# Kernel optimization log

Hardware: AMD Instinct MI355X
Metric: run time of the kernel (lower is better)

Reference implementation:

```python
import jax, jax.numpy as jnp
import numpy as np

N = 100000       # nodes
DEG = 16         # in-degree per node
E = N * DEG      # edges
IN_DIM = 128
H_DIM = 128
NEG_SLOPE = 0.01  # F.leaky_relu default


def setup_inputs() -> dict:
    key = jax.random.key(0)
    ks = jax.random.split(key, 12)
    sc = 0.05
    attr = jax.random.normal(ks[0], (N, IN_DIM), jnp.float32)
    edge_d = jax.random.uniform(ks[1], (E, 1), dtype=jnp.float32)
    edge_src = jax.random.randint(ks[2], (E,), 0, N, dtype=jnp.int32)
    edge_dst = jnp.repeat(jnp.arange(N, dtype=jnp.int32), DEG)  # every node gets DEG msgs
    return {
        "attr": attr,
        "edge_d": edge_d,
        "W_V1": jax.random.normal(ks[3], (1, 1), jnp.float32) * sc,
        "W_W1": jax.random.normal(ks[4], (H_DIM, IN_DIM), jnp.float32) * sc,
        "W_U1": jax.random.normal(ks[5], (H_DIM, IN_DIM), jnp.float32) * sc,
        "W_a1": jax.random.normal(ks[6], (1, 2 * H_DIM + 1), jnp.float32) * sc,
        "W_V2": jax.random.normal(ks[7], (1, 1), jnp.float32) * sc,
        "W_W2": jax.random.normal(ks[8], (H_DIM, H_DIM), jnp.float32) * sc,
        "W_U2": jax.random.normal(ks[9], (H_DIM, H_DIM), jnp.float32) * sc,
        "W_a2": jax.random.normal(ks[10], (1, 2 * H_DIM + 1), jnp.float32) * sc,
        "edge_src": edge_src,
        "edge_dst": edge_dst,
    }


def gat_layer(h, edge_d, edge_src, edge_dst, W_V, W_W, W_U, W_a):
    n = h.shape[0]
    t = edge_d @ W_V.T                      # [E,1] edge feature transform (fcV)
    z = h @ W_W.T                           # [N,H] (fcW)
    z_i = h @ W_U.T                         # [N,H] (fcU)
    Hd = z.shape[1]
    a = W_a[0]                              # [2H+1]
    a_src, a_dst, a_t = a[:Hd], a[Hd:2 * Hd], a[2 * Hd:]
    # attn_fc(concat(z_src, z_dst, t)) decomposed into per-node scores + edge term
    s_src = z @ a_src                       # [N]
    s_dst = z @ a_dst                       # [N]
    e = s_src[edge_src] + s_dst[edge_dst] + (t @ a_t)  # [E]
    e = jax.nn.leaky_relu(e, NEG_SLOPE)
    # per-destination-node softmax over incoming edges (mailbox softmax)
    m = jax.ops.segment_max(e, edge_dst, num_segments=n)
    ex = jnp.exp(e - m[edge_dst])
    denom = jax.ops.segment_sum(ex, edge_dst, num_segments=n)
    alpha = ex / denom[edge_dst]            # [E]
    # weighted neighbor aggregation
    zn = jax.ops.segment_sum(alpha[:, None] * z[edge_src], edge_dst, num_segments=n)
    return jax.nn.relu(z_i + zn)


def reference(attr, edge_d, W_V1, W_W1, W_U1, W_a1, W_V2, W_W2, W_U2, W_a2,
              edge_src, edge_dst):
    h = gat_layer(attr, edge_d, edge_src, edge_dst, W_V1, W_W1, W_U1, W_a1)
    h = gat_layer(h, edge_d, edge_src, edge_dst, W_V2, W_W2, W_U2, W_a2)
    return h
```

## Files before the change

### kernel.cpp

```cpp
#include <hip/hip_runtime.h>

#define N_NODES 100000
#define DEG 16
#define DIM 128
#define NTILES 1563
#define T8 196
#define DGRID (T8 * 4 * 8)
#define LSTR 136

typedef short bf16x8 __attribute__((ext_vector_type(8)));
typedef float f32x4 __attribute__((ext_vector_type(4)));

__device__ __forceinline__ unsigned short f2bf(float f) {
    unsigned int u = __builtin_bit_cast(unsigned int, f);
    u = (u + 0x7fffu + ((u >> 16) & 1u)) >> 16;
    return (unsigned short)u;
}
__device__ __forceinline__ float bf2f(unsigned short h) {
    unsigned int u = ((unsigned int)h) << 16;
    return __builtin_bit_cast(float, u);
}
__device__ __forceinline__ bf16x8 pack_bf16x8(float4 lo, float4 hi) {
    bf16x8 f;
    f[0] = (short)f2bf(lo.x); f[1] = (short)f2bf(lo.y);
    f[2] = (short)f2bf(lo.z); f[3] = (short)f2bf(lo.w);
    f[4] = (short)f2bf(hi.x); f[5] = (short)f2bf(hi.y);
    f[6] = (short)f2bf(hi.z); f[7] = (short)f2bf(hi.w);
    return f;
}

__global__ __launch_bounds__(256) void prep_w(
    const float* __restrict__ W_W1, const float* __restrict__ W_U1,
    const float* __restrict__ W_W2, const float* __restrict__ W_U2,
    unsigned short* __restrict__ Wc1, unsigned short* __restrict__ Wc2)
{
    int idx = blockIdx.x * 256 + threadIdx.x;
    int half = idx & 32767;
    const float* src = (idx < 32768)
        ? (half < 16384 ? W_W1 + half : W_U1 + half - 16384)
        : (half < 16384 ? W_W2 + half : W_U2 + half - 16384);
    unsigned short* dst = (idx < 32768) ? Wc1 + half : Wc2 + half;
    *dst = f2bf(*src);
}

__global__ __launch_bounds__(256, 4) void dense_tile(
    const float* __restrict__ hsrc,
    const unsigned short* __restrict__ Wc,
    const float* __restrict__ W_a,
    unsigned short* __restrict__ z,
    unsigned short* __restrict__ zi,
    float* __restrict__ s_src0, float* __restrict__ s_src1,
    float* __restrict__ s_dst0, float* __restrict__ s_dst1)
{
    __shared__ unsigned short Wt[64 * LSTR];
    __shared__ unsigned short Ht[64 * LSTR];

    const int bid = blockIdx.x;
    const int xcd = bid & 7;
    const int q = bid >> 3;
    const int cb = q & 3;
    const int tile = (q >> 2) * 8 + xcd;
    if (tile >= NTILES) return;
    const int nodebase = tile * 64;
    const int t = threadIdx.x;

    {
        int r = t >> 2, c0 = (t & 3) * 32;
        const unsigned short* src = Wc + (size_t)(cb * 64 + r) * DIM + c0;
        unsigned short* dst = Wt + r * LSTR + c0;
#pragma unroll
        for (int i = 0; i < 4; i++)
            *(uint4*)(dst + i * 8) = *(const uint4*)(src + i * 8);
    }
    {
        int r = t >> 2, c0 = (t & 3) * 32;
        int node = nodebase + r;
        unsigned short* dst = Ht + r * LSTR + c0;
        float4 v[8];
#pragma unroll
        for (int i = 0; i < 8; i++) v[i] = make_float4(0.f, 0.f, 0.f, 0.f);
        if (node < N_NODES) {
            const float* src = hsrc + (size_t)node * DIM + c0;
#pragma unroll
            for (int i = 0; i < 8; i++) v[i] = *(const float4*)(src + i * 4);
        }
#pragma unroll
        for (int i = 0; i < 4; i++)
            *(bf16x8*)(dst + i * 8) = pack_bf16x8(v[2 * i], v[2 * i + 1]);
    }
    __syncthreads();

    const int wave = t >> 6;
    const int lane = t & 63;
    const int n16 = lane & 15;
    const int quad = lane >> 4;
    const int node = nodebase + wave * 16 + n16;

    bf16x8 hfrag[4];
    const unsigned short* hrow = Ht + (wave * 16 + n16) * LSTR + quad * 8;
#pragma unroll
    for (int ks = 0; ks < 4; ks++)
        hfrag[ks] = *(const bf16x8*)(hrow + ks * 32);

    f32x4 acc[4];
#pragma unroll
    for (int ct = 0; ct < 4; ct++) {
        const unsigned short* wrow = Wt + (ct * 16 + n16) * LSTR + quad * 8;
        f32x4 a = {0.f, 0.f, 0.f, 0.f};
#pragma unroll
        for (int ks = 0; ks < 4; ks++)
            a = __builtin_amdgcn_mfma_f32_16x16x32_bf16(
                    *(const bf16x8*)(wrow + ks * 32), hfrag[ks], a, 0, 0, 0);
        acc[ct] = a;
    }

    if (node < N_NODES) {
        unsigned short* zout = (cb < 2 ? z : zi);
        unsigned short* orow = zout + (size_t)node * DIM + (cb & 1) * 64 + quad * 4;
#pragma unroll
        for (int ct = 0; ct < 4; ct++) {
            uint2 pk;
            pk.x = (unsigned int)f2bf(acc[ct][0]) | ((unsigned int)f2bf(acc[ct][1]) << 16);
            pk.y = (unsigned int)f2bf(acc[ct][2]) | ((unsigned int)f2bf(acc[ct][3]) << 16);
            *(uint2*)(orow + ct * 16) = pk;
        }
    }

    if (cb < 2) {
        float ps = 0.f, pd = 0.f;
#pragma unroll
        for (int ct = 0; ct < 4; ct++) {
            float4 as = *(const float4*)(W_a + cb * 64 + ct * 16 + quad * 4);
            float4 ad = *(const float4*)(W_a + DIM + cb * 64 + ct * 16 + quad * 4);
            ps += acc[ct][0] * as.x + acc[ct][1] * as.y
                + acc[ct][2] * as.z + acc[ct][3] * as.w;
            pd += acc[ct][0] * ad.x + acc[ct][1] * ad.y
                + acc[ct][2] * ad.z + acc[ct][3] * ad.w;
        }
        ps += __shfl_xor(ps, 16); ps += __shfl_xor(ps, 32);
        pd += __shfl_xor(pd, 16); pd += __shfl_xor(pd, 32);
        if (lane < 16 && node < N_NODES) {
            (cb == 0 ? s_src0 : s_src1)[node] = ps;
            (cb == 0 ? s_dst0 : s_dst1)[node] = pd;
        }
    }
}

__global__ __launch_bounds__(256, 3) void aggr_dense(
    const unsigned short* __restrict__ z,
    const unsigned short* __restrict__ zi,
    const float* __restrict__ s_src0, const float* __restrict__ s_src1,
    const float* __restrict__ s_dst0, const float* __restrict__ s_dst1,
    const float* __restrict__ edge_d,
    const int* __restrict__ edge_src,
    const float* __restrict__ W_V,
    const float* __restrict__ W_a,
    const unsigned short* __restrict__ Wc2,
    const float* __restrict__ W_a2,
    unsigned short* __restrict__ z2,
    unsigned short* __restrict__ zi2,
    float* __restrict__ t_src0, float* __restrict__ t_src1,
    float* __restrict__ t_dst0, float* __restrict__ t_dst1)
{
    __shared__ float alpha_s[16][DEG];
    __shared__ int   src_s[16][DEG];
    __shared__ unsigned short Hl[16 * LSTR];

    const int t = threadIdx.x;
    const int base = blockIdx.x * 16;

    {
        int nl = t >> 4, j = t & 15;
        int node = base + nl;
        int e = node * DEG + j;
        int s = edge_src[e];
        float coef = W_V[0] * W_a[2 * DIM];
        float x = (s_src0[s] + s_src1[s]) + (s_dst0[node] + s_dst1[node])
                + edge_d[e] * coef;
        x = x > 0.f ? x : 0.01f * x;
        float m = x;
        m = fmaxf(m, __shfl_xor(m, 1));
        m = fmaxf(m, __shfl_xor(m, 2));
        m = fmaxf(m, __shfl_xor(m, 4));
        m = fmaxf(m, __shfl_xor(m, 8));
        float ex = __expf(x - m);
        float d = ex;
        d += __shfl_xor(d, 1); d += __shfl_xor(d, 2);
        d += __shfl_xor(d, 4); d += __shfl_xor(d, 8);
        alpha_s[nl][j] = ex / d;
        src_s[nl][j] = s;
    }
    __syncthreads();

    {
        const int nl = t >> 4;
        const int node = base + nl;
        const int c8 = (t & 15) * 8;

        uint4 raw[DEG];
#pragma unroll
        for (int j = 0; j < DEG; j++)
            raw[j] = *(const uint4*)(z + (size_t)src_s[nl][j] * DIM + c8);
        uint4 zr = *(const uint4*)(zi + (size_t)node * DIM + c8);

        float acc[8] = {};
#pragma unroll
        for (int j = 0; j < DEG; j++) {
            float a = alpha_s[nl][j];
            acc[0] += a * bf2f((unsigned short)raw[j].x);
            acc[1] += a * bf2f((unsigned short)(raw[j].x >> 16));
            acc[2] += a * bf2f((unsigned short)raw[j].y);
            acc[3] += a * bf2f((unsigned short)(raw[j].y >> 16));
            acc[4] += a * bf2f((unsigned short)raw[j].z);
            acc[5] += a * bf2f((unsigned short)(raw[j].z >> 16));
            acc[6] += a * bf2f((unsigned short)raw[j].w);
            acc[7] += a * bf2f((unsigned short)(raw[j].w >> 16));
        }

        float v[8];
        v[0] = fmaxf(bf2f((unsigned short)zr.x) + acc[0], 0.f);
        v[1] = fmaxf(bf2f((unsigned short)(zr.x >> 16)) + acc[1], 0.f);
        v[2] = fmaxf(bf2f((unsigned short)zr.y) + acc[2], 0.f);
        v[3] = fmaxf(bf2f((unsigned short)(zr.y >> 16)) + acc[3], 0.f);
        v[4] = fmaxf(bf2f((unsigned short)zr.z) + acc[4], 0.f);
        v[5] = fmaxf(bf2f((unsigned short)(zr.z >> 16)) + acc[5], 0.f);
        v[6] = fmaxf(bf2f((unsigned short)zr.w) + acc[6], 0.f);
        v[7] = fmaxf(bf2f((unsigned short)(zr.w >> 16)) + acc[7], 0.f);

        uint4 pk;
        pk.x = (unsigned int)f2bf(v[0]) | ((unsigned int)f2bf(v[1]) << 16);
        pk.y = (unsigned int)f2bf(v[2]) | ((unsigned int)f2bf(v[3]) << 16);
        pk.z = (unsigned int)f2bf(v[4]) | ((unsigned int)f2bf(v[5]) << 16);
        pk.w = (unsigned int)f2bf(v[6]) | ((unsigned int)f2bf(v[7]) << 16);
        *(uint4*)(Hl + nl * LSTR + c8) = pk;
    }
    __syncthreads();

    const int wave = t >> 6;
    const int lane = t & 63;
    const int n16 = lane & 15;
    const int quad = lane >> 4;
    const int node = base + n16;

    bf16x8 hfrag[4];
    const unsigned short* hrow = Hl + n16 * LSTR + quad * 8;
#pragma unroll
    for (int ks = 0; ks < 4; ks++)
        hfrag[ks] = *(const bf16x8*)(hrow + ks * 32);

    f32x4 acc[4];
#pragma unroll
    for (int ct = 0; ct < 4; ct++) {
        const unsigned short* wrow = Wc2 + (size_t)(wave * 64 + ct * 16 + n16) * DIM + quad * 8;
        f32x4 a = {0.f, 0.f, 0.f, 0.f};
#pragma unroll
        for (int ks = 0; ks < 4; ks++)
            a = __builtin_amdgcn_mfma_f32_16x16x32_bf16(
                    *(const bf16x8*)(wrow + ks * 32), hfrag[ks], a, 0, 0, 0);
        acc[ct] = a;
    }

    {
        unsigned short* zout = (wave < 2 ? z2 : zi2);
        unsigned short* orow = zout + (size_t)node * DIM + (wave & 1) * 64 + quad * 4;
#pragma unroll
        for (int ct = 0; ct < 4; ct++) {
            uint2 pk;
            pk.x = (unsigned int)f2bf(acc[ct][0]) | ((unsigned int)f2bf(acc[ct][1]) << 16);
            pk.y = (unsigned int)f2bf(acc[ct][2]) | ((unsigned int)f2bf(acc[ct][3]) << 16);
            *(uint2*)(orow + ct * 16) = pk;
        }
    }

    if (wave < 2) {
        float ps = 0.f, pd = 0.f;
#pragma unroll
        for (int ct = 0; ct < 4; ct++) {
            float4 as = *(const float4*)(W_a2 + wave * 64 + ct * 16 + quad * 4);
            float4 ad = *(const float4*)(W_a2 + DIM + wave * 64 + ct * 16 + quad * 4);
            ps += acc[ct][0] * as.x + acc[ct][1] * as.y
                + acc[ct][2] * as.z + acc[ct][3] * as.w;
            pd += acc[ct][0] * ad.x + acc[ct][1] * ad.y
                + acc[ct][2] * ad.z + acc[ct][3] * ad.w;
        }
        ps += __shfl_xor(ps, 16); ps += __shfl_xor(ps, 32);
        pd += __shfl_xor(pd, 16); pd += __shfl_xor(pd, 32);
        if (lane < 16) {
            (wave == 0 ? t_src0 : t_src1)[node] = ps;
            (wave == 0 ? t_dst0 : t_dst1)[node] = pd;
        }
    }
}

__global__ __launch_bounds__(256, 3) void aggr_final(
    const unsigned short* __restrict__ z,
    const unsigned short* __restrict__ zi,
    const float* __restrict__ s_src0, const float* __restrict__ s_src1,
    const float* __restrict__ s_dst0, const float* __restrict__ s_dst1,
    const float* __restrict__ edge_d,
    const int* __restrict__ edge_src,
    const float* __restrict__ W_V,
    const float* __restrict__ W_a,
    float* __restrict__ out_f32)
{
    __shared__ float alpha_s[16][DEG];
    __shared__ int   src_s[16][DEG];

    const int t = threadIdx.x;
    const int base = blockIdx.x * 16;

    {
        int nl = t >> 4, j = t & 15;
        int node = base + nl;
        int e = node * DEG + j;
        int s = edge_src[e];
        float coef = W_V[0] * W_a[2 * DIM];
        float x = (s_src0[s] + s_src1[s]) + (s_dst0[node] + s_dst1[node])
                + edge_d[e] * coef;
        x = x > 0.f ? x : 0.01f * x;
        float m = x;
        m = fmaxf(m, __shfl_xor(m, 1));
        m = fmaxf(m, __shfl_xor(m, 2));
        m = fmaxf(m, __shfl_xor(m, 4));
        m = fmaxf(m, __shfl_xor(m, 8));
        float ex = __expf(x - m);
        float d = ex;
        d += __shfl_xor(d, 1); d += __shfl_xor(d, 2);
        d += __shfl_xor(d, 4); d += __shfl_xor(d, 8);
        alpha_s[nl][j] = ex / d;
        src_s[nl][j] = s;
    }
    __syncthreads();

    const int nl = t >> 4;
    const int node = base + nl;
    const int c8 = (t & 15) * 8;

    uint4 raw[DEG];
#pragma unroll
    for (int j = 0; j < DEG; j++)
        raw[j] = *(const uint4*)(z + (size_t)src_s[nl][j] * DIM + c8);
    uint4 zr = *(const uint4*)(zi + (size_t)node * DIM + c8);

    float acc[8] = {};
#pragma unroll
    for (int j = 0; j < DEG; j++) {
        float a = alpha_s[nl][j];
        acc[0] += a * bf2f((unsigned short)raw[j].x);
        acc[1] += a * bf2f((unsigned short)(raw[j].x >> 16));
        acc[2] += a * bf2f((unsigned short)raw[j].y);
        acc[3] += a * bf2f((unsigned short)(raw[j].y >> 16));
        acc[4] += a * bf2f((unsigned short)raw[j].z);
        acc[5] += a * bf2f((unsigned short)(raw[j].z >> 16));
        acc[6] += a * bf2f((unsigned short)raw[j].w);
        acc[7] += a * bf2f((unsigned short)(raw[j].w >> 16));
    }

    float* op = out_f32 + (size_t)node * DIM + c8;
    *(float4*)op = make_float4(
        fmaxf(bf2f((unsigned short)zr.x) + acc[0], 0.f),
        fmaxf(bf2f((unsigned short)(zr.x >> 16)) + acc[1], 0.f),
        fmaxf(bf2f((unsigned short)zr.y) + acc[2], 0.f),
        fmaxf(bf2f((unsigned short)(zr.y >> 16)) + acc[3], 0.f));
    *(float4*)(op + 4) = make_float4(
        fmaxf(bf2f((unsigned short)zr.z) + acc[4], 0.f),
        fmaxf(bf2f((unsigned short)(zr.z >> 16)) + acc[5], 0.f),
        fmaxf(bf2f((unsigned short)zr.w) + acc[6], 0.f),
        fmaxf(bf2f((unsigned short)(zr.w >> 16)) + acc[7], 0.f));
}

extern "C" void kernel_launch(void* const* d_in, const int* in_sizes, int n_in,
                              void* d_out, int out_size, void* d_ws, size_t ws_size,
                              hipStream_t stream) {
    const float* attr     = (const float*)d_in[0];
    const float* edge_d   = (const float*)d_in[1];
    const float* W_V1     = (const float*)d_in[2];
    const float* W_W1     = (const float*)d_in[3];
    const float* W_U1     = (const float*)d_in[4];
    const float* W_a1     = (const float*)d_in[5];
    const float* W_V2     = (const float*)d_in[6];
    const float* W_W2     = (const float*)d_in[7];
    const float* W_U2     = (const float*)d_in[8];
    const float* W_a2     = (const float*)d_in[9];
    const int*   edge_src = (const int*)d_in[10];

    float* out = (float*)d_out;

    char* ws = (char*)d_ws;
    unsigned short* z1  = (unsigned short*)ws;
    unsigned short* zi1 = (unsigned short*)(ws + 26u * 1024 * 1024);
    unsigned short* z2  = (unsigned short*)(ws + 52u * 1024 * 1024);
    unsigned short* zi2 = (unsigned short*)(ws + 78u * 1024 * 1024);
    unsigned short* Wc1 = (unsigned short*)(ws + 104u * 1024 * 1024);
    unsigned short* Wc2 = (unsigned short*)(ws + 105u * 1024 * 1024);
    float* s_src0       = (float*)(ws + 106u * 1024 * 1024);
    float* s_src1       = (float*)(ws + 107u * 1024 * 1024);
    float* s_dst0       = (float*)(ws + 108u * 1024 * 1024);
    float* s_dst1       = (float*)(ws + 109u * 1024 * 1024);
    float* t_src0       = (float*)(ws + 110u * 1024 * 1024);
    float* t_src1       = (float*)(ws + 111u * 1024 * 1024);
    float* t_dst0       = (float*)(ws + 112u * 1024 * 1024);
    float* t_dst1       = (float*)(ws + 113u * 1024 * 1024);

    prep_w<<<256, 256, 0, stream>>>(W_W1, W_U1, W_W2, W_U2, Wc1, Wc2);

    dense_tile<<<DGRID, 256, 0, stream>>>(attr, Wc1, W_a1, z1, zi1,
                                          s_src0, s_src1, s_dst0, s_dst1);

    aggr_dense<<<6250, 256, 0, stream>>>(z1, zi1, s_src0, s_src1, s_dst0, s_dst1,
                                         edge_d, edge_src, W_V1, W_a1,
                                         Wc2, W_a2, z2, zi2,
                                         t_src0, t_src1, t_dst0, t_dst1);

    aggr_final<<<6250, 256, 0, stream>>>(z2, zi2, t_src0, t_src1, t_dst0, t_dst1,
                                         edge_d, edge_src, W_V2, W_a2, out);
}
```

Measured before the change: 326.0 us.

## Issue neighbor gathers before softmax using wave shuffles instead of LDS staging

In both aggregation kernels, the per-edge source indices and softmax weights are now passed between lanes with wave shuffles rather than written to shared memory behind a block barrier. The 16 neighbor-row gathers and the self-row load are issued right after the edge indices are read, and a scheduling barrier keeps them ahead of the attention-score and softmax arithmetic so that arithmetic runs while the loads are in flight. This removes the shared-memory round trip and one __syncthreads per block. In exchange, each thread keeps more registers live across the softmax, which could lower occupancy.

```diff
diff --git a/kernel.cpp b/kernel.cpp
--- a/kernel.cpp
+++ b/kernel.cpp
@@ -162,71 +162,75 @@
     float* __restrict__ t_src0, float* __restrict__ t_src1,
     float* __restrict__ t_dst0, float* __restrict__ t_dst1)
 {
-    __shared__ float alpha_s[16][DEG];
-    __shared__ int   src_s[16][DEG];
     __shared__ unsigned short Hl[16 * LSTR];
 
     const int t = threadIdx.x;
     const int base = blockIdx.x * 16;
+    const int nl = t >> 4;
+    const int j  = t & 15;
+    const int nodej = base + nl;
+    const int lane = t & 63;
+    const int gb = lane & 48;
+
+    const int e = nodej * DEG + j;
+
+    int   s  = edge_src[e];
+    float ed = edge_d[e];
+
+    float v_ss0 = s_src0[s];
+    float v_ss1 = s_src1[s];
+    float v_sd0 = s_dst0[nodej];
+    float v_sd1 = s_dst1[nodej];
+
+    const int c8 = j * 8;
+    uint4 raw[DEG];
+#pragma unroll
+    for (int jj = 0; jj < DEG; jj++) {
+        int sj = __shfl(s, gb | jj);
+        raw[jj] = *(const uint4*)(z + (size_t)sj * DIM + c8);
+    }
+    uint4 zr = *(const uint4*)(zi + (size_t)nodej * DIM + c8);
+    __builtin_amdgcn_sched_barrier(0);
+
+    float coef = W_V[0] * W_a[2 * DIM];
+    float x = (v_ss0 + v_ss1) + (v_sd0 + v_sd1) + ed * coef;
+    x = x > 0.f ? x : 0.01f * x;
+    float m = x;
+    m = fmaxf(m, __shfl_xor(m, 1));
+    m = fmaxf(m, __shfl_xor(m, 2));
+    m = fmaxf(m, __shfl_xor(m, 4));
+    m = fmaxf(m, __shfl_xor(m, 8));
+    float ex = __expf(x - m);
+    float d = ex;
+    d += __shfl_xor(d, 1); d += __shfl_xor(d, 2);
+    d += __shfl_xor(d, 4); d += __shfl_xor(d, 8);
+    float aj = ex / d;
+
+    float acc8[8] = {};
+#pragma unroll
+    for (int jj = 0; jj < DEG; jj++) {
+        float a = __shfl(aj, gb | jj);
+        acc8[0] += a * bf2f((unsigned short)raw[jj].x);
+        acc8[1] += a * bf2f((unsigned short)(raw[jj].x >> 16));
+        acc8[2] += a * bf2f((unsigned short)raw[jj].y);
+        acc8[3] += a * bf2f((unsigned short)(raw[jj].y >> 16));
+        acc8[4] += a * bf2f((unsigned short)raw[jj].z);
+        acc8[5] += a * bf2f((unsigned short)(raw[jj].z >> 16));
+        acc8[6] += a * bf2f((unsigned short)raw[jj].w);
+        acc8[7] += a * bf2f((unsigned short)(raw[jj].w >> 16));
+    }
+
+    float v[8];
+    v[0] = fmaxf(bf2f((unsigned short)zr.x) + acc8[0], 0.f);
+    v[1] = fmaxf(bf2f((unsigned short)(zr.x >> 16)) + acc8[1], 0.f);
+    v[2] = fmaxf(bf2f((unsigned short)zr.y) + acc8[2], 0.f);
+    v[3] = fmaxf(bf2f((unsigned short)(zr.y >> 16)) + acc8[3], 0.f);
+    v[4] = fmaxf(bf2f((unsigned short)zr.z) + acc8[4], 0.f);
+    v[5] = fmaxf(bf2f((unsigned short)(zr.z >> 16)) + acc8[5], 0.f);
+    v[6] = fmaxf(bf2f((unsigned short)zr.w) + acc8[6], 0.f);
+    v[7] = fmaxf(bf2f((unsigned short)(zr.w >> 16)) + acc8[7], 0.f);
 
     {
-        int nl = t >> 4, j = t & 15;
-        int node = base + nl;
-        int e = node * DEG + j;
-        int s = edge_src[e];
-        float coef = W_V[0] * W_a[2 * DIM];
-        float x = (s_src0[s] + s_src1[s]) + (s_dst0[node] + s_dst1[node])
-                + edge_d[e] * coef;
-        x = x > 0.f ? x : 0.01f * x;
-        float m = x;
-        m = fmaxf(m, __shfl_xor(m, 1));
-        m = fmaxf(m, __shfl_xor(m, 2));
-        m = fmaxf(m, __shfl_xor(m, 4));
-        m = fmaxf(m, __shfl_xor(m, 8));
-        float ex = __expf(x - m);
-        float d = ex;
-        d += __shfl_xor(d, 1); d += __shfl_xor(d, 2);
-        d += __shfl_xor(d, 4); d += __shfl_xor(d, 8);
-        alpha_s[nl][j] = ex / d;
-        src_s[nl][j] = s;
-    }
-    __syncthreads();
-
-    {
-        const int nl = t >> 4;
-        const int node = base + nl;
-        const int c8 = (t & 15) * 8;
-
-        uint4 raw[DEG];
-#pragma unroll
-        for (int j = 0; j < DEG; j++)
-            raw[j] = *(const uint4*)(z + (size_t)src_s[nl][j] * DIM + c8);
-        uint4 zr = *(const uint4*)(zi + (size_t)node * DIM + c8);
-
-        float acc[8] = {};
-#pragma unroll
-        for (int j = 0; j < DEG; j++) {
-            float a = alpha_s[nl][j];
-            acc[0] += a * bf2f((unsigned short)raw[j].x);
-            acc[1] += a * bf2f((unsigned short)(raw[j].x >> 16));
-            acc[2] += a * bf2f((unsigned short)raw[j].y);
-            acc[3] += a * bf2f((unsigned short)(raw[j].y >> 16));
-            acc[4] += a * bf2f((unsigned short)raw[j].z);
-            acc[5] += a * bf2f((unsigned short)(raw[j].z >> 16));
-            acc[6] += a * bf2f((unsigned short)raw[j].w);
-            acc[7] += a * bf2f((unsigned short)(raw[j].w >> 16));
-        }
-
-        float v[8];
-        v[0] = fmaxf(bf2f((unsigned short)zr.x) + acc[0], 0.f);
-        v[1] = fmaxf(bf2f((unsigned short)(zr.x >> 16)) + acc[1], 0.f);
-        v[2] = fmaxf(bf2f((unsigned short)zr.y) + acc[2], 0.f);
-        v[3] = fmaxf(bf2f((unsigned short)(zr.y >> 16)) + acc[3], 0.f);
-        v[4] = fmaxf(bf2f((unsigned short)zr.z) + acc[4], 0.f);
-        v[5] = fmaxf(bf2f((unsigned short)(zr.z >> 16)) + acc[5], 0.f);
-        v[6] = fmaxf(bf2f((unsigned short)zr.w) + acc[6], 0.f);
-        v[7] = fmaxf(bf2f((unsigned short)(zr.w >> 16)) + acc[7], 0.f);
-
         uint4 pk;
         pk.x = (unsigned int)f2bf(v[0]) | ((unsigned int)f2bf(v[1]) << 16);
         pk.y = (unsigned int)f2bf(v[2]) | ((unsigned int)f2bf(v[3]) << 16);
@@ -237,7 +241,6 @@
     __syncthreads();
 
     const int wave = t >> 6;
-    const int lane = t & 63;
     const int n16 = lane & 15;
     const int quad = lane >> 4;
     const int node = base + n16;
@@ -303,57 +306,60 @@
     const float* __restrict__ W_a,
     float* __restrict__ out_f32)
 {
-    __shared__ float alpha_s[16][DEG];
-    __shared__ int   src_s[16][DEG];
-
     const int t = threadIdx.x;
     const int base = blockIdx.x * 16;
-
-    {
-        int nl = t >> 4, j = t & 15;
-        int node = base + nl;
-        int e = node * DEG + j;
-        int s = edge_src[e];
-        float coef = W_V[0] * W_a[2 * DIM];
-        float x = (s_src0[s] + s_src1[s]) + (s_dst0[node] + s_dst1[node])
-                + edge_d[e] * coef;
-        x = x > 0.f ? x : 0.01f * x;
-        float m = x;
-        m = fmaxf(m, __shfl_xor(m, 1));
-        m = fmaxf(m, __shfl_xor(m, 2));
-        m = fmaxf(m, __shfl_xor(m, 4));
-        m = fmaxf(m, __shfl_xor(m, 8));
-        float ex = __expf(x - m);
-        float d = ex;
-        d += __shfl_xor(d, 1); d += __shfl_xor(d, 2);
-        d += __shfl_xor(d, 4); d += __shfl_xor(d, 8);
-        alpha_s[nl][j] = ex / d;
-        src_s[nl][j] = s;
-    }
-    __syncthreads();
-
     const int nl = t >> 4;
+    const int j  = t & 15;
     const int node = base + nl;
-    const int c8 = (t & 15) * 8;
-
+    const int lane = t & 63;
+    const int gb = lane & 48;
+
+    const int e = node * DEG + j;
+
+    int   s  = edge_src[e];
+    float ed = edge_d[e];
+
+    float v_ss0 = s_src0[s];
+    float v_ss1 = s_src1[s];
+    float v_sd0 = s_dst0[node];
+    float v_sd1 = s_dst1[node];
+
+    const int c8 = j * 8;
     uint4 raw[DEG];
 #pragma unroll
-    for (int j = 0; j < DEG; j++)
-        raw[j] = *(const uint4*)(z + (size_t)src_s[nl][j] * DIM + c8);
+    for (int jj = 0; jj < DEG; jj++) {
+        int sj = __shfl(s, gb | jj);
+        raw[jj] = *(const uint4*)(z + (size_t)sj * DIM + c8);
+    }
     uint4 zr = *(const uint4*)(zi + (size_t)node * DIM + c8);
+    __builtin_amdgcn_sched_barrier(0);
+
+    float coef = W_V[0] * W_a[2 * DIM];
+    float x = (v_ss0 + v_ss1) + (v_sd0 + v_sd1) + ed * coef;
+    x = x > 0.f ? x : 0.01f * x;
+    float m = x;
+    m = fmaxf(m, __shfl_xor(m, 1));
+    m = fmaxf(m, __shfl_xor(m, 2));
+    m = fmaxf(m, __shfl_xor(m, 4));
+    m = fmaxf(m, __shfl_xor(m, 8));
+    float ex = __expf(x - m);
+    float d = ex;
+    d += __shfl_xor(d, 1); d += __shfl_xor(d, 2);
+    d += __shfl_xor(d, 4); d += __shfl_xor(d, 8);
+    float aj = ex / d;
 
     float acc[8] = {};
 #pragma unroll
-    for (int j = 0; j < DEG; j++) {
-        float a = alpha_s[nl][j];
-        acc[0] += a * bf2f((unsigned short)raw[j].x);
-        acc[1] += a * bf2f((unsigned short)(raw[j].x >> 16));
-        acc[2] += a * bf2f((unsigned short)raw[j].y);
-        acc[3] += a * bf2f((unsigned short)(raw[j].y >> 16));
-        acc[4] += a * bf2f((unsigned short)raw[j].z);
-        acc[5] += a * bf2f((unsigned short)(raw[j].z >> 16));
-        acc[6] += a * bf2f((unsigned short)raw[j].w);
-        acc[7] += a * bf2f((unsigned short)(raw[j].w >> 16));
+    for (int jj = 0; jj < DEG; jj++) {
+        float a = __shfl(aj, gb | jj);
+        acc[0] += a * bf2f((unsigned short)raw[jj].x);
+        acc[1] += a * bf2f((unsigned short)(raw[jj].x >> 16));
+        acc[2] += a * bf2f((unsigned short)raw[jj].y);
+        acc[3] += a * bf2f((unsigned short)(raw[jj].y >> 16));
+        acc[4] += a * bf2f((unsigned short)raw[jj].z);
+        acc[5] += a * bf2f((unsigned short)(raw[jj].z >> 16));
+        acc[6] += a * bf2f((unsigned short)raw[jj].w);
+        acc[7] += a * bf2f((unsigned short)(raw[jj].w >> 16));
     }
 
     float* op = out_f32 + (size_t)node * DIM + c8;
```

Result: no change. 320.0 us (-1.8%).

## Split aggregation into alpha kernel and column-sliced gather, unfuse layer-2 GEMM

Applied to the files above, without the earlier changes.

Replaces the fused aggregate+GEMM kernels with a separate per-edge softmax kernel that writes alpha to memory, a gather kernel where each block handles one 16-column slice of 64 nodes, and a standalone bf16 MFMA GEMM for layer 2. The column slicing, with slice taken from the low bits of blockIdx, is meant to keep each slice of z resident in a smaller cache footprint and raise parallelism for the random gathers. The cost is more launches and extra round-trips to memory for alpha and h1. Launch-bounds occupancy hints are also dropped.

```diff
diff --git a/kernel.cpp b/kernel.cpp
--- a/kernel.cpp
+++ b/kernel.cpp
@@ -3,9 +3,11 @@
 #define N_NODES 100000
 #define DEG 16
 #define DIM 128
+#define E_EDGES 1600000
 #define NTILES 1563
 #define T8 196
 #define DGRID (T8 * 4 * 8)
+#define CHUNKS 1563
 #define LSTR 136
 
 typedef short bf16x8 __attribute__((ext_vector_type(8)));
@@ -43,7 +45,7 @@
     *dst = f2bf(*src);
 }
 
-__global__ __launch_bounds__(256, 4) void dense_tile(
+__global__ __launch_bounds__(256) void dense_tile(
     const float* __restrict__ hsrc,
     const unsigned short* __restrict__ Wc,
     const float* __restrict__ W_a,
@@ -146,227 +148,258 @@
     }
 }
 
-__global__ __launch_bounds__(256, 3) void aggr_dense(
-    const unsigned short* __restrict__ z,
-    const unsigned short* __restrict__ zi,
+__global__ __launch_bounds__(256) void dense_tile_b(
+    const unsigned short* __restrict__ hsrc,
+    const unsigned short* __restrict__ Wc,
+    const float* __restrict__ W_a,
+    unsigned short* __restrict__ z,
+    unsigned short* __restrict__ zi,
+    float* __restrict__ s_src0, float* __restrict__ s_src1,
+    float* __restrict__ s_dst0, float* __restrict__ s_dst1)
+{
+    __shared__ unsigned short Wt[64 * LSTR];
+    __shared__ unsigned short Ht[64 * LSTR];
+
+    const int bid = blockIdx.x;
+    const int xcd = bid & 7;
+    const int q = bid >> 3;
+    const int cb = q & 3;
+    const int tile = (q >> 2) * 8 + xcd;
+    if (tile >= NTILES) return;
+    const int nodebase = tile * 64;
+    const int t = threadIdx.x;
+
+    {
+        int r = t >> 2, c0 = (t & 3) * 32;
+        const unsigned short* src = Wc + (size_t)(cb * 64 + r) * DIM + c0;
+        unsigned short* dst = Wt + r * LSTR + c0;
+#pragma unroll
+        for (int i = 0; i < 4; i++)
+            *(uint4*)(dst + i * 8) = *(const uint4*)(src + i * 8);
+    }
+    {
+        int r = t >> 2, c0 = (t & 3) * 32;
+        int node = nodebase + r;
+        unsigned short* dst = Ht + r * LSTR + c0;
+        if (node < N_NODES) {
+            const unsigned short* src = hsrc + (size_t)node * DIM + c0;
+#pragma unroll
+            for (int i = 0; i < 4; i++)
+                *(uint4*)(dst + i * 8) = *(const uint4*)(src + i * 8);
+        } else {
+            uint4 zr4 = make_uint4(0, 0, 0, 0);
+#pragma unroll
+            for (int i = 0; i < 4; i++) *(uint4*)(dst + i * 8) = zr4;
+        }
+    }
+    __syncthreads();
+
+    const int wave = t >> 6;
+    const int lane = t & 63;
+    const int n16 = lane & 15;
+    const int quad = lane >> 4;
+    const int node = nodebase + wave * 16 + n16;
+
+    bf16x8 hfrag[4];
+    const unsigned short* hrow = Ht + (wave * 16 + n16) * LSTR + quad * 8;
+#pragma unroll
+    for (int ks = 0; ks < 4; ks++)
+        hfrag[ks] = *(const bf16x8*)(hrow + ks * 32);
+
+    f32x4 acc[4];
+#pragma unroll
+    for (int ct = 0; ct < 4; ct++) {
+        const unsigned short* wrow = Wt + (ct * 16 + n16) * LSTR + quad * 8;
+        f32x4 a = {0.f, 0.f, 0.f, 0.f};
+#pragma unroll
+        for (int ks = 0; ks < 4; ks++)
+            a = __builtin_amdgcn_mfma_f32_16x16x32_bf16(
+                    *(const bf16x8*)(wrow + ks * 32), hfrag[ks], a, 0, 0, 0);
+        acc[ct] = a;
+    }
+
+    if (node < N_NODES) {
+        unsigned short* zout = (cb < 2 ? z : zi);
+        unsigned short* orow = zout + (size_t)node * DIM + (cb & 1) * 64 + quad * 4;
+#pragma unroll
+        for (int ct = 0; ct < 4; ct++) {
+            uint2 pk;
+            pk.x = (unsigned int)f2bf(acc[ct][0]) | ((unsigned int)f2bf(acc[ct][1]) << 16);
+            pk.y = (unsigned int)f2bf(acc[ct][2]) | ((unsigned int)f2bf(acc[ct][3]) << 16);
+            *(uint2*)(orow + ct * 16) = pk;
+        }
+    }
+
+    if (cb < 2) {
+        float ps = 0.f, pd = 0.f;
+#pragma unroll
+        for (int ct = 0; ct < 4; ct++) {
+            float4 as = *(const float4*)(W_a + cb * 64 + ct * 16 + quad * 4);
+            float4 ad = *(const float4*)(W_a + DIM + cb * 64 + ct * 16 + quad * 4);
+            ps += acc[ct][0] * as.x + acc[ct][1] * as.y
+                + acc[ct][2] * as.z + acc[ct][3] * as.w;
+            pd += acc[ct][0] * ad.x + acc[ct][1] * ad.y
+                + acc[ct][2] * ad.z + acc[ct][3] * ad.w;
+        }
+        ps += __shfl_xor(ps, 16); ps += __shfl_xor(ps, 32);
+        pd += __shfl_xor(pd, 16); pd += __shfl_xor(pd, 32);
+        if (lane < 16 && node < N_NODES) {
+            (cb == 0 ? s_src0 : s_src1)[node] = ps;
+            (cb == 0 ? s_dst0 : s_dst1)[node] = pd;
+        }
+    }
+}
+
+__global__ __launch_bounds__(256) void alpha_k(
     const float* __restrict__ s_src0, const float* __restrict__ s_src1,
     const float* __restrict__ s_dst0, const float* __restrict__ s_dst1,
     const float* __restrict__ edge_d,
     const int* __restrict__ edge_src,
     const float* __restrict__ W_V,
     const float* __restrict__ W_a,
-    const unsigned short* __restrict__ Wc2,
-    const float* __restrict__ W_a2,
-    unsigned short* __restrict__ z2,
-    unsigned short* __restrict__ zi2,
-    float* __restrict__ t_src0, float* __restrict__ t_src1,
-    float* __restrict__ t_dst0, float* __restrict__ t_dst1)
-{
-    __shared__ float alpha_s[16][DEG];
-    __shared__ int   src_s[16][DEG];
-    __shared__ unsigned short Hl[16 * LSTR];
-
-    const int t = threadIdx.x;
-    const int base = blockIdx.x * 16;
-
-    {
-        int nl = t >> 4, j = t & 15;
-        int node = base + nl;
-        int e = node * DEG + j;
-        int s = edge_src[e];
-        float coef = W_V[0] * W_a[2 * DIM];
-        float x = (s_src0[s] + s_src1[s]) + (s_dst0[node] + s_dst1[node])
-                + edge_d[e] * coef;
-        x = x > 0.f ? x : 0.01f * x;
-        float m = x;
-        m = fmaxf(m, __shfl_xor(m, 1));
-        m = fmaxf(m, __shfl_xor(m, 2));
-        m = fmaxf(m, __shfl_xor(m, 4));
-        m = fmaxf(m, __shfl_xor(m, 8));
-        float ex = __expf(x - m);
-        float d = ex;
-        d += __shfl_xor(d, 1); d += __shfl_xor(d, 2);
-        d += __shfl_xor(d, 4); d += __shfl_xor(d, 8);
-        alpha_s[nl][j] = ex / d;
-        src_s[nl][j] = s;
-    }
-    __syncthreads();
-
-    {
-        const int nl = t >> 4;
-        const int node = base + nl;
-        const int c8 = (t & 15) * 8;
-
-        uint4 raw[DEG];
-#pragma unroll
-        for (int j = 0; j < DEG; j++)
-            raw[j] = *(const uint4*)(z + (size_t)src_s[nl][j] * DIM + c8);
-        uint4 zr = *(const uint4*)(zi + (size_t)node * DIM + c8);
-
-        float acc[8] = {};
-#pragma unroll
-        for (int j = 0; j < DEG; j++) {
-            float a = alpha_s[nl][j];
-            acc[0] += a * bf2f((unsigned short)raw[j].x);
-            acc[1] += a * bf2f((unsigned short)(raw[j].x >> 16));
-            acc[2] += a * bf2f((unsigned short)raw[j].y);
-            acc[3] += a * bf2f((unsigned short)(raw[j].y >> 16));
-            acc[4] += a * bf2f((unsigned short)raw[j].z);
-            acc[5] += a * bf2f((unsigned short)(raw[j].z >> 16));
-            acc[6] += a * bf2f((unsigned short)raw[j].w);
-            acc[7] += a * bf2f((unsigned short)(raw[j].w >> 16));
-        }
-
-        float v[8];
-        v[0] = fmaxf(bf2f((unsigned short)zr.x) + acc[0], 0.f);
-        v[1] = fmaxf(bf2f((unsigned short)(zr.x >> 16)) + acc[1], 0.f);
-        v[2] = fmaxf(bf2f((unsigned short)zr.y) + acc[2], 0.f);
-        v[3] = fmaxf(bf2f((unsigned short)(zr.y >> 16)) + acc[3], 0.f);
-        v[4] = fmaxf(bf2f((unsigned short)zr.z) + acc[4], 0.f);
-        v[5] = fmaxf(bf2f((unsigned short)(zr.z >> 16)) + acc[5], 0.f);
-        v[6] = fmaxf(bf2f((unsigned short)zr.w) + acc[6], 0.f);
-        v[7] = fmaxf(bf2f((unsigned short)(zr.w >> 16)) + acc[7], 0.f);
-
-        uint4 pk;
-        pk.x = (unsigned int)f2bf(v[0]) | ((unsigned int)f2bf(v[1]) << 16);
-        pk.y = (unsigned int)f2bf(v[2]) | ((unsigned int)f2bf(v[3]) << 16);
-        pk.z = (unsigned int)f2bf(v[4]) | ((unsigned int)f2bf(v[5]) << 16);
-        pk.w = (unsigned int)f2bf(v[6]) | ((unsigned int)f2bf(v[7]) << 16);
-        *(uint4*)(Hl + nl * LSTR + c8) = pk;
-    }
-    __syncthreads();
-
-    const int wave = t >> 6;
-    const int lane = t & 63;
-    const int n16 = lane & 15;
-    const int quad = lane >> 4;
-    const int node = base + n16;
-
-    bf16x8 hfrag[4];
-    const unsigned short* hrow = Hl + n16 * LSTR + quad * 8;
-#pragma unroll
-    for (int ks = 0; ks < 4; ks++)
-        hfrag[ks] = *(const bf16x8*)(hrow + ks * 32);
-
-    f32x4 acc[4];
-#pragma unroll
-    for (int ct = 0; ct < 4; ct++) {
-        const unsigned short* wrow = Wc2 + (size_t)(wave * 64 + ct * 16 + n16) * DIM + quad * 8;
-        f32x4 a = {0.f, 0.f, 0.f, 0.f};
-#pragma unroll
-        for (int ks = 0; ks < 4; ks++)
-            a = __builtin_amdgcn_mfma_f32_16x16x32_bf16(
-                    *(const bf16x8*)(wrow + ks * 32), hfrag[ks], a, 0, 0, 0);
-        acc[ct] = a;
-    }
-
-    {
-        unsigned short* zout = (wave < 2 ? z2 : zi2);
-        unsigned short* orow = zout + (size_t)node * DIM + (wave & 1) * 64 + quad * 4;
-#pragma unroll
-        for (int ct = 0; ct < 4; ct++) {
-            uint2 pk;
-            pk.x = (unsigned int)f2bf(acc[ct][0]) | ((unsigned int)f2bf(acc[ct][1]) << 16);
-            pk.y = (unsigned int)f2bf(acc[ct][2]) | ((unsigned int)f2bf(acc[ct][3]) << 16);
-            *(uint2*)(orow + ct * 16) = pk;
-        }
-    }
-
-    if (wave < 2) {
-        float ps = 0.f, pd = 0.f;
-#pragma unroll
-        for (int ct = 0; ct < 4; ct++) {
-            float4 as = *(const float4*)(W_a2 + wave * 64 + ct * 16 + quad * 4);
-            float4 ad = *(const float4*)(W_a2 + DIM + wave * 64 + ct * 16 + quad * 4);
-            ps += acc[ct][0] * as.x + acc[ct][1] * as.y
-                + acc[ct][2] * as.z + acc[ct][3] * as.w;
-            pd += acc[ct][0] * ad.x + acc[ct][1] * ad.y
-                + acc[ct][2] * ad.z + acc[ct][3] * ad.w;
-        }
-        ps += __shfl_xor(ps, 16); ps += __shfl_xor(ps, 32);
-        pd += __shfl_xor(pd, 16); pd += __shfl_xor(pd, 32);
-        if (lane < 16) {
-            (wave == 0 ? t_src0 : t_src1)[node] = ps;
-            (wave == 0 ? t_dst0 : t_dst1)[node] = pd;
-        }
-    }
-}
-
-__global__ __launch_bounds__(256, 3) void aggr_final(
+    float* __restrict__ alpha)
+{
+    const int e = blockIdx.x * 256 + threadIdx.x;
+    const int node = e >> 4;
+    int   s  = edge_src[e];
+    float ed = edge_d[e];
+    float coef = W_V[0] * W_a[2 * DIM];
+    float x = (s_src0[s] + s_src1[s]) + (s_dst0[node] + s_dst1[node]) + ed * coef;
+    x = x > 0.f ? x : 0.01f * x;
+    float m = x;
+    m = fmaxf(m, __shfl_xor(m, 1));
+    m = fmaxf(m, __shfl_xor(m, 2));
+    m = fmaxf(m, __shfl_xor(m, 4));
+    m = fmaxf(m, __shfl_xor(m, 8));
+    float ex = __expf(x - m);
+    float d = ex;
+    d += __shfl_xor(d, 1); d += __shfl_xor(d, 2);
+    d += __shfl_xor(d, 4); d += __shfl_xor(d, 8);
+    alpha[e] = ex / d;
+}
+
+__global__ __launch_bounds__(256) void aggr_slice(
     const unsigned short* __restrict__ z,
     const unsigned short* __restrict__ zi,
-    const float* __restrict__ s_src0, const float* __restrict__ s_src1,
-    const float* __restrict__ s_dst0, const float* __restrict__ s_dst1,
-    const float* __restrict__ edge_d,
+    const float* __restrict__ alpha,
     const int* __restrict__ edge_src,
-    const float* __restrict__ W_V,
-    const float* __restrict__ W_a,
+    unsigned short* __restrict__ hout)
+{
+    __shared__ float alpha_s[64][17];
+    __shared__ int   src_s[64][17];
+
+    const int bid = blockIdx.x;
+    const int slice = bid & 7;
+    const int chunk = bid >> 3;
+    const int t = threadIdx.x;
+    const int nodebase = chunk * 64;
+
+    {
+        int idx = t * 4;
+        int e0 = nodebase * DEG + idx;
+        int nl = idx >> 4, j0 = idx & 15;
+        float4 a4 = make_float4(0.f, 0.f, 0.f, 0.f);
+        int4   s4 = make_int4(0, 0, 0, 0);
+        if (e0 < E_EDGES) {
+            a4 = *(const float4*)(alpha + e0);
+            s4 = *(const int4*)(edge_src + e0);
+        }
+        alpha_s[nl][j0 + 0] = a4.x; alpha_s[nl][j0 + 1] = a4.y;
+        alpha_s[nl][j0 + 2] = a4.z; alpha_s[nl][j0 + 3] = a4.w;
+        src_s[nl][j0 + 0] = s4.x; src_s[nl][j0 + 1] = s4.y;
+        src_s[nl][j0 + 2] = s4.z; src_s[nl][j0 + 3] = s4.w;
+    }
+    __syncthreads();
+
+    const int nl  = t >> 2;
+    const int col = slice * 16 + (t & 3) * 4;
+    const int node = nodebase + nl;
+    const unsigned short* zcol = z + col;
+
+    float a0 = 0.f, a1 = 0.f, a2 = 0.f, a3 = 0.f;
+#pragma unroll
+    for (int e = 0; e < DEG; e++) {
+        int   sj = src_s[nl][e];
+        float a  = alpha_s[nl][e];
+        uint2 r = *(const uint2*)(zcol + (size_t)sj * DIM);
+        a0 += a * bf2f((unsigned short)(r.x & 0xffff));
+        a1 += a * bf2f((unsigned short)(r.x >> 16));
+        a2 += a * bf2f((unsigned short)(r.y & 0xffff));
+        a3 += a * bf2f((unsigned short)(r.y >> 16));
+    }
+
+    if (node < N_NODES) {
+        uint2 zr = *(const uint2*)(zi + (size_t)node * DIM + col);
+        float v0 = fmaxf(bf2f((unsigned short)(zr.x & 0xffff)) + a0, 0.f);
+        float v1 = fmaxf(bf2f((unsigned short)(zr.x >> 16)) + a1, 0.f);
+        float v2 = fmaxf(bf2f((unsigned short)(zr.y & 0xffff)) + a2, 0.f);
+        float v3 = fmaxf(bf2f((unsigned short)(zr.y >> 16)) + a3, 0.f);
+        uint2 pk;
+        pk.x = (unsigned int)f2bf(v0) | ((unsigned int)f2bf(v1) << 16);
+        pk.y = (unsigned int)f2bf(v2) | ((unsigned int)f2bf(v3) << 16);
+        *(uint2*)(hout + (size_t)node * DIM + col) = pk;
+    }
+}
+
+__global__ __launch_bounds__(256) void aggr_slice_final(
+    const unsigned short* __restrict__ z,
+    const unsigned short* __restrict__ zi,
+    const float* __restrict__ alpha,
+    const int* __restrict__ edge_src,
     float* __restrict__ out_f32)
 {
-    __shared__ float alpha_s[16][DEG];
-    __shared__ int   src_s[16][DEG];
-
+    __shared__ float alpha_s[64][17];
+    __shared__ int   src_s[64][17];
+
+    const int bid = blockIdx.x;
+    const int slice = bid & 7;
+    const int chunk = bid >> 3;
     const int t = threadIdx.x;
-    const int base = blockIdx.x * 16;
-
-    {
-        int nl = t >> 4, j = t & 15;
-        int node = base + nl;
-        int e = node * DEG + j;
-        int s = edge_src[e];
-        float coef = W_V[0] * W_a[2 * DIM];
-        float x = (s_src0[s] + s_src1[s]) + (s_dst0[node] + s_dst1[node])
-                + edge_d[e] * coef;
-        x = x > 0.f ? x : 0.01f * x;
-        float m = x;
-        m = fmaxf(m, __shfl_xor(m, 1));
-        m = fmaxf(m, __shfl_xor(m, 2));
-        m = fmaxf(m, __shfl_xor(m, 4));
-        m = fmaxf(m, __shfl_xor(m, 8));
-        float ex = __expf(x - m);
-        float d = ex;
-        d += __shfl_xor(d, 1); d += __shfl_xor(d, 2);
-        d += __shfl_xor(d, 4); d += __shfl_xor(d, 8);
-        alpha_s[nl][j] = ex / d;
-        src_s[nl][j] = s;
+    const int nodebase = chunk * 64;
+
+    {
+        int idx = t * 4;
+        int e0 = nodebase * DEG + idx;
+        int nl = idx >> 4, j0 = idx & 15;
+        float4 a4 = make_float4(0.f, 0.f, 0.f, 0.f);
+        int4   s4 = make_int4(0, 0, 0, 0);
+        if (e0 < E_EDGES) {
+            a4 = *(const float4*)(alpha + e0);
+            s4 = *(const int4*)(edge_src + e0);
+        }
+        alpha_s[nl][j0 + 0] = a4.x; alpha_s[nl][j0 + 1] = a4.y;
+        alpha_s[nl][j0 + 2] = a4.z; alpha_s[nl][j0 + 3] = a4.w;
+        src_s[nl][j0 + 0] = s4.x; src_s[nl][j0 + 1] = s4.y;
+        src_s[nl][j0 + 2] = s4.z; src_s[nl][j0 + 3] = s4.w;
     }
     __syncthreads();
 
-    const int nl = t >> 4;
-    const int node = base + nl;
-    const int c8 = (t & 15) * 8;
-
-    uint4 raw[DEG];
-#pragma unroll
-    for (int j = 0; j < DEG; j++)
-        raw[j] = *(const uint4*)(z + (size_t)src_s[nl][j] * DIM + c8);
-    uint4 zr = *(const uint4*)(zi + (size_t)node * DIM + c8);
-
-    float acc[8] = {};
-#pragma unroll
-    for (int j = 0; j < DEG; j++) {
-        float a = alpha_s[nl][j];
-        acc[0] += a * bf2f((unsigned short)raw[j].x);
-        acc[1] += a * bf2f((unsigned short)(raw[j].x >> 16));
-        acc[2] += a * bf2f((unsigned short)raw[j].y);
-        acc[3] += a * bf2f((unsigned short)(raw[j].y >> 16));
-        acc[4] += a * bf2f((unsigned short)raw[j].z);
-        acc[5] += a * bf2f((unsigned short)(raw[j].z >> 16));
-        acc[6] += a * bf2f((unsigned short)raw[j].w);
-        acc[7] += a * bf2f((unsigned short)(raw[j].w >> 16));
-    }
-
-    float* op = out_f32 + (size_t)node * DIM + c8;
-    *(float4*)op = make_float4(
-        fmaxf(bf2f((unsigned short)zr.x) + acc[0], 0.f),
-        fmaxf(bf2f((unsigned short)(zr.x >> 16)) + acc[1], 0.f),
-        fmaxf(bf2f((unsigned short)zr.y) + acc[2], 0.f),
-        fmaxf(bf2f((unsigned short)(zr.y >> 16)) + acc[3], 0.f));
-    *(float4*)(op + 4) = make_float4(
-        fmaxf(bf2f((unsigned short)zr.z) + acc[4], 0.f),
-        fmaxf(bf2f((unsigned short)(zr.z >> 16)) + acc[5], 0.f),
-        fmaxf(bf2f((unsigned short)zr.w) + acc[6], 0.f),
-        fmaxf(bf2f((unsigned short)(zr.w >> 16)) + acc[7], 0.f));
+    const int nl  = t >> 2;
+    const int col = slice * 16 + (t & 3) * 4;
+    const int node = nodebase + nl;
+    const unsigned short* zcol = z + col;
+
+    float a0 = 0.f, a1 = 0.f, a2 = 0.f, a3 = 0.f;
+#pragma unroll
+    for (int e = 0; e < DEG; e++) {
+        int   sj = src_s[nl][e];
+        float a  = alpha_s[nl][e];
+        uint2 r = *(const uint2*)(zcol + (size_t)sj * DIM);
+        a0 += a * bf2f((unsigned short)(r.x & 0xffff));
+        a1 += a * bf2f((unsigned short)(r.x >> 16));
+        a2 += a * bf2f((unsigned short)(r.y & 0xffff));
+        a3 += a * bf2f((unsigned short)(r.y >> 16));
+    }
+
+    if (node < N_NODES) {
+        uint2 zr = *(const uint2*)(zi + (size_t)node * DIM + col);
+        f32x4 o;
+        o[0] = fmaxf(bf2f((unsigned short)(zr.x & 0xffff)) + a0, 0.f);
+        o[1] = fmaxf(bf2f((unsigned short)(zr.x >> 16)) + a1, 0.f);
+        o[2] = fmaxf(bf2f((unsigned short)(zr.y & 0xffff)) + a2, 0.f);
+        o[3] = fmaxf(bf2f((unsigned short)(zr.y >> 16)) + a3, 0.f);
+        *(f32x4*)(out_f32 + (size_t)node * DIM + col) = o;
+    }
 }
 
 extern "C" void kernel_launch(void* const* d_in, const int* in_sizes, int n_in,
@@ -387,31 +420,34 @@
     float* out = (float*)d_out;
 
     char* ws = (char*)d_ws;
-    unsigned short* z1  = (unsigned short*)ws;
-    unsigned short* zi1 = (unsigned short*)(ws + 26u * 1024 * 1024);
-    unsigned short* z2  = (unsigned short*)(ws + 52u * 1024 * 1024);
-    unsigned short* zi2 = (unsigned short*)(ws + 78u * 1024 * 1024);
-    unsigned short* Wc1 = (unsigned short*)(ws + 104u * 1024 * 1024);
-    unsigned short* Wc2 = (unsigned short*)(ws + 105u * 1024 * 1024);
-    float* s_src0       = (float*)(ws + 106u * 1024 * 1024);
-    float* s_src1       = (float*)(ws + 107u * 1024 * 1024);
-    float* s_dst0       = (float*)(ws + 108u * 1024 * 1024);
-    float* s_dst1       = (float*)(ws + 109u * 1024 * 1024);
-    float* t_src0       = (float*)(ws + 110u * 1024 * 1024);
-    float* t_src1       = (float*)(ws + 111u * 1024 * 1024);
-    float* t_dst0       = (float*)(ws + 112u * 1024 * 1024);
-    float* t_dst1       = (float*)(ws + 113u * 1024 * 1024);
+    unsigned short* z1    = (unsigned short*)ws;
+    unsigned short* zi1   = (unsigned short*)(ws + 26u * 1024 * 1024);
+    unsigned short* h1    = (unsigned short*)(ws + 52u * 1024 * 1024);
+    unsigned short* Wc1   = (unsigned short*)(ws + 78u * 1024 * 1024);
+    unsigned short* Wc2   = (unsigned short*)(ws + 79u * 1024 * 1024);
+    float* s_src0         = (float*)(ws + 80u * 1024 * 1024);
+    float* s_src1         = (float*)(ws + 81u * 1024 * 1024);
+    float* s_dst0         = (float*)(ws + 82u * 1024 * 1024);
+    float* s_dst1         = (float*)(ws + 83u * 1024 * 1024);
+    float* alphaA         = (float*)(ws + 84u * 1024 * 1024);
+    unsigned short* z2  = z1;
+    unsigned short* zi2 = zi1;
 
     prep_w<<<256, 256, 0, stream>>>(W_W1, W_U1, W_W2, W_U2, Wc1, Wc2);
 
     dense_tile<<<DGRID, 256, 0, stream>>>(attr, Wc1, W_a1, z1, zi1,
                                           s_src0, s_src1, s_dst0, s_dst1);
 
-    aggr_dense<<<6250, 256, 0, stream>>>(z1, zi1, s_src0, s_src1, s_dst0, s_dst1,
-                                         edge_d, edge_src, W_V1, W_a1,
-                                         Wc2, W_a2, z2, zi2,
-                                         t_src0, t_src1, t_dst0, t_dst1);
-
-    aggr_final<<<6250, 256, 0, stream>>>(z2, zi2, t_src0, t_src1, t_dst0, t_dst1,
-                                         edge_d, edge_src, W_V2, W_a2, out);
-}
+    alpha_k<<<6250, 256, 0, stream>>>(s_src0, s_src1, s_dst0, s_dst1,
+                                      edge_d, edge_src, W_V1, W_a1, alphaA);
+
+    aggr_slice<<<CHUNKS * 8, 256, 0, stream>>>(z1, zi1, alphaA, edge_src, h1);
+
+    dense_tile_b<<<DGRID, 256, 0, stream>>>(h1, Wc2, W_a2, z2, zi2,
+                                            s_src0, s_src1, s_dst0, s_dst1);
+
+    alpha_k<<<6250, 256, 0, stream>>>(s_src0, s_src1, s_dst0, s_dst1,
+                                      edge_d, edge_src, W_V2, W_a2, alphaA);
+
+    aggr_slice_final<<<CHUNKS * 8, 256, 0, stream>>>(z2, zi2, alphaA, edge_src, out);
+}
```

Measured after the change: 621.3 us. 1.91x slower.
